# Performance work log

Hardware: AMD Instinct MI355X
Metric: run time of the kernel (lower is better)

Reference implementation:

```python
import jax, jax.numpy as jnp
import numpy as np
import math

EPS = 1e-5


def _layernorm(x, gamma, beta):
    mu = jnp.mean(x, axis=-1, keepdims=True)
    var = jnp.var(x, axis=-1, keepdims=True)
    return (x - mu) * jax.lax.rsqrt(var + EPS) * gamma + beta


def _quantum_head(x, theta_rx):
    # RX(x_i) then RX(theta_i) on wire i == RX(x_i + theta_i); product state,
    # CNOT ring is a Z-basis permutation => <Z_j> = prod_{i in S_j} cos(a_i)
    # with S_j = {0..j} for j>=1 (chain of CNOT(i,i+1)) and S_0 = {1..7}
    # (final CNOT(7,0) makes b0 = b1^...^b7).
    c = jnp.cos(x + theta_rx)                       # (B,S,8)
    cp = jnp.cumprod(c, axis=-1)                    # prefix products c0..cj
    z0 = jnp.prod(c[..., 1:], axis=-1, keepdims=True)
    return jnp.concatenate([z0, cp[..., 1:]], axis=-1)  # (B,S,8)


def _quantum_ffn(x, theta_ry):
    # RX(x_i) |0>, then RY(theta_i), measure Z: <Z_i> = cos(theta_i) * cos(x_i)
    return jnp.cos(theta_ry) * jnp.cos(x)


def setup_inputs() -> dict:
    key = jax.random.key(0)
    ks = jax.random.split(key, 6)
    B, S, E, F = 16, 2048, 8, 512
    return {
        'x': jax.random.normal(ks[0], (B, S, E), jnp.float32),
        'theta_rx': jax.random.normal(ks[1], (E,), jnp.float32),
        'w_out': jax.random.normal(ks[2], (E, E), jnp.float32) / math.sqrt(E),
        'theta_ry': jax.random.normal(ks[3], (E,), jnp.float32),
        'w1': jax.random.normal(ks[4], (F, E), jnp.float32) / math.sqrt(E),
        'b1': jnp.zeros((F,), jnp.float32),
        'w2': jax.random.normal(ks[5], (E, F), jnp.float32) / math.sqrt(F),
        'b2': jnp.zeros((E,), jnp.float32),
        'gamma1': jnp.ones((E,), jnp.float32),
        'beta1': jnp.zeros((E,), jnp.float32),
        'gamma2': jnp.ones((E,), jnp.float32),
        'beta2': jnp.zeros((E,), jnp.float32),
    }


def reference(x, theta_rx, w_out, theta_ry, w1, b1, w2, b2,
              gamma1, beta1, gamma2, beta2):
    B, S, E = x.shape
    H = 2
    D = E // H
    # --- quantum multi-head attention (shared head => q == k == v) ---
    z = _quantum_head(x, theta_rx)                       # (B,S,E)
    qh = z.reshape(B, S, H, D).transpose(0, 2, 1, 3)     # (B,H,S,D)
    scores = jnp.einsum('bhqd,bhkd->bhqk', qh, qh) / math.sqrt(D)
    attn = jax.nn.softmax(scores, axis=-1)
    out = jnp.einsum('bhqk,bhkd->bhqd', attn, qh)        # (B,H,S,D)
    out = out.transpose(0, 2, 1, 3).reshape(B, S, E)
    attn_out = out @ w_out.T                             # out_proj, no bias
    x1 = _layernorm(x + attn_out, gamma1, beta1)
    # --- quantum feed-forward ---
    zf = _quantum_ffn(x1, theta_ry)                      # (B,S,E)
    h = zf @ w1.T + b1                                   # (B,S,F)
    ffn_out = jax.nn.relu(h) @ w2.T + b2                 # (B,S,E)
    return _layernorm(x1 + ffn_out, gamma2, beta2)
```

## Files before the change

### kernel.cpp

```cpp
#include <hip/hip_runtime.h>
#include <math.h>
#include <utility>

#define NB 16
#define NS 2048
#define NE 8
#define NH 2
#define NF 512
#define DEG 6
#define NMONO 210
#define KPB 64
#define NCHUNK 32
#define PHI_LD 66
#define QPB 128
#define LNEPS 1e-5f
#define PART_STRIDE (5 * NMONO)

typedef float f32x2 __attribute__((ext_vector_type(2)));
typedef _Float16 h2 __attribute__((ext_vector_type(2)));

#if defined(__has_builtin)
# if __has_builtin(__builtin_amdgcn_fdot2)
#  define FDOT2(a,b,c) __builtin_amdgcn_fdot2((a),(b),(c),false)
# endif
#endif
#ifndef FDOT2
static __device__ __forceinline__ float fdot2_sw(h2 a, h2 b, float c) {
    return c + (float)a.x * (float)b.x + (float)a.y * (float)b.y;
}
# define FDOT2(a,b,c) fdot2_sw((a),(b),(c))
#endif

constexpr float ACOEF_C[7] = {0.99994459f, 2.00308514f, 2.00174650f,
                              1.30890404f, 0.65803033f, 0.31441604f, 0.10241921f};

constexpr int mono_e(int idx) {
    int i = 0;
    for (int e0 = 0; e0 <= DEG; ++e0)
        for (int e1 = 0; e1 <= DEG - e0; ++e1)
            for (int e2 = 0; e2 <= DEG - e0 - e1; ++e2)
                for (int e3 = 0; e3 <= DEG - e0 - e1 - e2; ++e3) {
                    if (i == idx) return (e0 << 12) | (e1 << 8) | (e2 << 4) | e3;
                    ++i;
                }
    return 0;
}
constexpr float mfact(int n) { float r = 1.f; for (int i = 2; i <= n; ++i) r *= (float)i; return r; }
constexpr float mono_c(int idx) {
    const int E = mono_e(idx);
    const int e0 = E >> 12, e1 = (E >> 8) & 15, e2 = (E >> 4) & 15, e3 = E & 15;
    const int d = e0 + e1 + e2 + e3;
    return ACOEF_C[d] * (mfact(d) / (mfact(e0) * mfact(e1) * mfact(e2) * mfact(e3)));
}

template <int BEG, class F, int... Is>
__device__ __forceinline__ void sf_impl(F f, std::integer_sequence<int, Is...>) {
    (f(std::integral_constant<int, BEG + Is>{}), ...);
}
template <int BEG, int END, class F>
__device__ __forceinline__ void static_for(F f) {
    sf_impl<BEG>(f, std::make_integer_sequence<int, END - BEG>{});
}

template <int BEG, int END>
__device__ __forceinline__ void phi_body(_Float16* __restrict__ Phi, int lane,
                                         const float (&pw0)[7], const float (&pw1)[7],
                                         const float (&pw2)[7], const float (&pw3)[7]) {
    static_for<BEG, END>([&](auto Ic) {
        constexpr int idx = Ic.value;
        constexpr int E = mono_e(idx);
        constexpr float C = mono_c(idx);
        const float v = C * (pw0[E >> 12] * pw1[(E >> 8) & 15]) *
                            (pw2[(E >> 4) & 15] * pw3[E & 15]);
        Phi[idx * PHI_LD + lane] = (_Float16)v;
    });
}

__global__ __launch_bounds__(256, 4)
void k1_moments(const float* __restrict__ x, const float* __restrict__ theta_rx,
                float* __restrict__ ws) {
    __shared__ _Float16 Phi[NMONO * PHI_LD];
    __shared__ __align__(16) _Float16 kvh[KPB / 2][8];
    __shared__ float th_s[8];

    const int t = threadIdx.x, bid = blockIdx.x;
    const int kc = bid & 31, h = (bid >> 5) & 1, b = bid >> 6;

    if (t < 8) th_s[t] = theta_rx[t];
    __syncthreads();

    const int lane = t & 63, wq = t >> 6;
    {
        const float* xr = x + ((size_t)b * NS + kc * KPB + lane) * NE;
        const float4 v0 = *reinterpret_cast<const float4*>(xr);
        const float4 v1 = *reinterpret_cast<const float4*>(xr + 4);
        const float c0 = __cosf(v0.x + th_s[0]), c1 = __cosf(v0.y + th_s[1]);
        const float c2 = __cosf(v0.z + th_s[2]), c3 = __cosf(v0.w + th_s[3]);
        const float c4 = __cosf(v1.x + th_s[4]), c5 = __cosf(v1.y + th_s[5]);
        const float c6 = __cosf(v1.z + th_s[6]), c7 = __cosf(v1.w + th_s[7]);
        const float p1 = c0*c1, p2 = p1*c2, p3 = p2*c3, p4 = p3*c4;
        const float p5 = p4*c5, p6 = p5*c6, p7 = p6*c7;
        float k0, k1v, k2v, k3v;
        if (h == 0) {
            const float s6 = c7*c6, s5 = s6*c5, s4 = s5*c4, s3 = s4*c3, s2 = s3*c2;
            k0 = s2*c1; k1v = p1; k2v = p2; k3v = p3;
        } else {
            k0 = p4; k1v = p5; k2v = p6; k3v = p7;
        }
        if (t < 64) {
            const int j = t >> 1, par = t & 1;
            kvh[j][0 + par] = (_Float16)k0;  kvh[j][2 + par] = (_Float16)k1v;
            kvh[j][4 + par] = (_Float16)k2v; kvh[j][6 + par] = (_Float16)k3v;
        }
        float pw0[7], pw1[7], pw2[7], pw3[7];
        pw0[0] = pw1[0] = pw2[0] = pw3[0] = 1.f;
        #pragma unroll
        for (int i = 1; i <= DEG; ++i) {
            pw0[i] = pw0[i-1] * k0;  pw1[i] = pw1[i-1] * k1v;
            pw2[i] = pw2[i-1] * k2v; pw3[i] = pw3[i-1] * k3v;
        }
        switch (wq) {
            case 0: phi_body<0,   53 >(Phi, lane, pw0, pw1, pw2, pw3); break;
            case 1: phi_body<53,  106>(Phi, lane, pw0, pw1, pw2, pw3); break;
            case 2: phi_body<106, 159>(Phi, lane, pw0, pw1, pw2, pw3); break;
            default: phi_body<159, 210>(Phi, lane, pw0, pw1, pw2, pw3); break;
        }
    }
    __syncthreads();

    if (t < NMONO) {
        const h2 one2 = {(_Float16)1.f, (_Float16)1.f};
        float a0 = 0.f, a1 = 0.f, a2 = 0.f, a3 = 0.f, a4 = 0.f;
        #pragma unroll 8
        for (int j = 0; j < KPB / 2; ++j) {
            const h2 phi2 = *reinterpret_cast<const h2*>(&Phi[t * PHI_LD + 2 * j]);
            const float4 kv4 = *reinterpret_cast<const float4*>(&kvh[j][0]);
            const h2 kA = __builtin_bit_cast(h2, kv4.x);
            const h2 kB = __builtin_bit_cast(h2, kv4.y);
            const h2 kC = __builtin_bit_cast(h2, kv4.z);
            const h2 kD = __builtin_bit_cast(h2, kv4.w);
            a0 = FDOT2(phi2, kA, a0);
            a1 = FDOT2(phi2, kB, a1);
            a2 = FDOT2(phi2, kC, a2);
            a3 = FDOT2(phi2, kD, a3);
            a4 = FDOT2(phi2, one2, a4);
        }
        float* dst = ws + (size_t)bid * PART_STRIDE;
        dst[0 * NMONO + t] = a0;
        dst[1 * NMONO + t] = a1;
        dst[2 * NMONO + t] = a2;
        dst[3 * NMONO + t] = a3;
        dst[4 * NMONO + t] = a4;
    }
}

template <int BEG, int END>
__device__ __forceinline__ void p2_body2(const float4* __restrict__ Mn,
                                         const float* __restrict__ Md, int base,
                                         const float (&pwA)[4][7], const float (&pwB)[4][7],
                                         f32x2& a01A, f32x2& a23A, float& adA,
                                         f32x2& a01B, f32x2& a23B, float& adB) {
    static_for<BEG, END>([&](auto Ic) {
        constexpr int idx = Ic.value;
        constexpr int E = mono_e(idx);
        constexpr int e0 = E >> 12, e1 = (E >> 8) & 15, e2 = (E >> 4) & 15, e3 = E & 15;
        const float4 mv = Mn[base + idx];
        const float  md = Md[base + idx];
        const f32x2 m01 = {mv.x, mv.y}, m23 = {mv.z, mv.w};
        const float PA = (pwA[0][e0] * pwA[1][e1]) * (pwA[2][e2] * pwA[3][e3]);
        const float PB = (pwB[0][e0] * pwB[1][e1]) * (pwB[2][e2] * pwB[3][e3]);
        a01A += PA * m01;  a23A += PA * m23;  adA += PA * md;
        a01B += PB * m01;  a23B += PB * m23;  adB += PB * md;
    });
}

__global__ __launch_bounds__(1024)
void k2_main(const float* __restrict__ x, const float* __restrict__ theta_rx,
             const float* __restrict__ w_out, const float* __restrict__ theta_ry,
             const float* __restrict__ w1, const float* __restrict__ b1,
             const float* __restrict__ w2, const float* __restrict__ b2,
             const float* __restrict__ g1, const float* __restrict__ be1,
             const float* __restrict__ g2, const float* __restrict__ be2,
             const float* __restrict__ ws, float* __restrict__ out) {
    __shared__ float4 Mn_lds[2 * NMONO];
    __shared__ float  Md_lds[2 * NMONO];
    __shared__ float  z_c[8][QPB];
    __shared__ float  x1_c[8][QPB];
    __shared__ float  zf_c[8][QPB];
    __shared__ float  attn_c[8][QPB];
    __shared__ float  part_a[4][256][5];
    __shared__ float  part_f[8][QPB][9];
    __shared__ float  w1_s[NF][NE];
    __shared__ float  w2t_s[NF][NE];
    __shared__ float  b1_s[NF];
    __shared__ float  wout_s[NE][NE];
    __shared__ float  th_s[8], cry_s[8], g1_s[8], be1_s[8], g2_s[8], be2_s[8], b2_s[8];

    const int t = threadIdx.x, bid = blockIdx.x;
    const int b = bid >> 4, qc = bid & 15;

    if (t < 2 * NMONO) {
        const int h = (t >= NMONO) ? 1 : 0;
        const int a = t - h * NMONO;
        const float* src = ws + (size_t)((b * 2 + h) * NCHUNK) * PART_STRIDE;
        float s0 = 0.f, s1 = 0.f, s2 = 0.f, s3 = 0.f, s4 = 0.f;
        #pragma unroll 4
        for (int kc = 0; kc < NCHUNK; ++kc) {
            const float* p = src + (size_t)kc * PART_STRIDE;
            s0 += p[0 * NMONO + a]; s1 += p[1 * NMONO + a];
            s2 += p[2 * NMONO + a]; s3 += p[3 * NMONO + a];
            s4 += p[4 * NMONO + a];
        }
        Mn_lds[t] = make_float4(s0, s1, s2, s3);
        Md_lds[t] = s4;
    }

    for (int i = t; i < NF * NE; i += 1024) {
        ((float*)w1_s)[i] = w1[i];
        const int e = i >> 9, f = i & (NF - 1);
        w2t_s[f][e] = w2[i];
    }
    if (t < NF) b1_s[t] = b1[t];
    if (t < NE * NE) ((float*)wout_s)[t] = w_out[t];
    if (t < 8) {
        th_s[t]  = theta_rx[t];
        cry_s[t] = __cosf(theta_ry[t]);
        g1_s[t]  = g1[t];  be1_s[t] = be1[t];
        g2_s[t]  = g2[t];  be2_s[t] = be2[t];
        b2_s[t]  = b2[t];
    }
    __syncthreads();

    if (t < QPB) {
        const float* xr = x + ((size_t)b * NS + qc * QPB + t) * NE;
        const float4 v0 = *reinterpret_cast<const float4*>(xr);
        const float4 v1 = *reinterpret_cast<const float4*>(xr + 4);
        const float c0 = __cosf(v0.x + th_s[0]), c1 = __cosf(v0.y + th_s[1]);
        const float c2 = __cosf(v0.z + th_s[2]), c3 = __cosf(v0.w + th_s[3]);
        const float c4 = __cosf(v1.x + th_s[4]), c5 = __cosf(v1.y + th_s[5]);
        const float c6 = __cosf(v1.z + th_s[6]), c7 = __cosf(v1.w + th_s[7]);
        const float p1 = c0*c1, p2 = p1*c2, p3 = p2*c3, p4 = p3*c4;
        const float p5 = p4*c5, p6 = p5*c6, p7 = p6*c7;
        const float s6 = c7*c6, s5 = s6*c5, s4 = s5*c4, s3 = s4*c3, s2 = s3*c2;
        z_c[0][t] = s2*c1; z_c[1][t] = p1; z_c[2][t] = p2; z_c[3][t] = p3;
        z_c[4][t] = p4;    z_c[5][t] = p5; z_c[6][t] = p6; z_c[7][t] = p7;
    }
    __syncthreads();

    if (t < 512) {
        const int w = t >> 6, l = t & 63;
        const int g = w >> 1, h = w & 1;
        const int rA = l, rB = l + 64;
        float pwA[4][7], pwB[4][7];
        #pragma unroll
        for (int d = 0; d < 4; ++d) {
            const float uA = z_c[h*4+d][rA] * 0.25f;
            const float uB = z_c[h*4+d][rB] * 0.25f;
            pwA[d][0] = 1.f; pwB[d][0] = 1.f;
            #pragma unroll
            for (int i = 1; i <= DEG; ++i) {
                pwA[d][i] = pwA[d][i-1] * uA;
                pwB[d][i] = pwB[d][i-1] * uB;
            }
        }
        f32x2 a01A = {0.f,0.f}, a23A = {0.f,0.f}, a01B = {0.f,0.f}, a23B = {0.f,0.f};
        float adA = 0.f, adB = 0.f;
        const int base = h * NMONO;
        switch (g) {
            case 0: p2_body2<0,   53 >(Mn_lds, Md_lds, base, pwA, pwB, a01A, a23A, adA, a01B, a23B, adB); break;
            case 1: p2_body2<53,  106>(Mn_lds, Md_lds, base, pwA, pwB, a01A, a23A, adA, a01B, a23B, adB); break;
            case 2: p2_body2<106, 159>(Mn_lds, Md_lds, base, pwA, pwB, a01A, a23A, adA, a01B, a23B, adB); break;
            default: p2_body2<159, 210>(Mn_lds, Md_lds, base, pwA, pwB, a01A, a23A, adA, a01B, a23B, adB); break;
        }
        float* pa = &part_a[g][h * 128 + rA][0];
        pa[0] = a01A.x; pa[1] = a01A.y; pa[2] = a23A.x; pa[3] = a23A.y; pa[4] = adA;
        float* pb = &part_a[g][h * 128 + rB][0];
        pb[0] = a01B.x; pb[1] = a01B.y; pb[2] = a23B.x; pb[3] = a23B.y; pb[4] = adB;
    }
    __syncthreads();

    if (t < 256) {
        const int h = t >> 7, r = t & 127;
        float n0 = 0.f, n1 = 0.f, n2 = 0.f, n3 = 0.f, dd = 0.f;
        #pragma unroll
        for (int g = 0; g < 4; ++g) {
            const float* pa = &part_a[g][t][0];
            n0 += pa[0]; n1 += pa[1]; n2 += pa[2]; n3 += pa[3]; dd += pa[4];
        }
        const float inv = 1.0f / dd;
        attn_c[h*4+0][r] = n0 * inv; attn_c[h*4+1][r] = n1 * inv;
        attn_c[h*4+2][r] = n2 * inv; attn_c[h*4+3][r] = n3 * inv;
    }
    __syncthreads();

    if (t < QPB) {
        float av[NE];
        #pragma unroll
        for (int e = 0; e < NE; ++e) av[e] = attn_c[e][t];
        float y[NE];
        #pragma unroll
        for (int e = 0; e < NE; ++e) {
            float acc = 0.f;
            #pragma unroll
            for (int k = 0; k < NE; ++k) acc += av[k] * wout_s[e][k];
            y[e] = acc;
        }
        const float* xr = x + ((size_t)b * NS + qc * QPB + t) * NE;
        const float4 xv0 = *reinterpret_cast<const float4*>(xr);
        const float4 xv1 = *reinterpret_cast<const float4*>(xr + 4);
        float t1[NE];
        t1[0] = xv0.x + y[0]; t1[1] = xv0.y + y[1]; t1[2] = xv0.z + y[2]; t1[3] = xv0.w + y[3];
        t1[4] = xv1.x + y[4]; t1[5] = xv1.y + y[5]; t1[6] = xv1.z + y[6]; t1[7] = xv1.w + y[7];
        float mu = 0.f;
        #pragma unroll
        for (int e = 0; e < NE; ++e) mu += t1[e];
        mu *= 0.125f;
        float var = 0.f;
        #pragma unroll
        for (int e = 0; e < NE; ++e) { const float d = t1[e] - mu; var += d * d; }
        var *= 0.125f;
        const float inv1 = rsqrtf(var + LNEPS);
        #pragma unroll
        for (int e = 0; e < NE; ++e) {
            const float x1e = (t1[e] - mu) * inv1 * g1_s[e] + be1_s[e];
            x1_c[e][t] = x1e;
            zf_c[e][t] = cry_s[e] * __cosf(x1e);
        }
    }
    __syncthreads();

    if (t < 256) {
        const int fs = t >> 5;
        const int rr = t & 31;
        f32x2 zf01[4], zf23[4], zf45[4], zf67[4];
        #pragma unroll
        for (int k = 0; k < 4; ++k) {
            const int row = rr + 32 * k;
            zf01[k] = (f32x2){zf_c[0][row], zf_c[1][row]};
            zf23[k] = (f32x2){zf_c[2][row], zf_c[3][row]};
            zf45[k] = (f32x2){zf_c[4][row], zf_c[5][row]};
            zf67[k] = (f32x2){zf_c[6][row], zf_c[7][row]};
        }
        f32x2 a01[4] = {}, a23[4] = {}, a45[4] = {}, a67[4] = {};
        #pragma unroll 4
        for (int i = 0; i < 64; ++i) {
            const int f = fs * 64 + i;
            const float4 wa = *reinterpret_cast<const float4*>(&w1_s[f][0]);
            const float4 wb = *reinterpret_cast<const float4*>(&w1_s[f][4]);
            const float bb = b1_s[f];
            const float4 ua = *reinterpret_cast<const float4*>(&w2t_s[f][0]);
            const float4 ub = *reinterpret_cast<const float4*>(&w2t_s[f][4]);
            const f32x2 wa01 = {wa.x, wa.y}, wa23 = {wa.z, wa.w};
            const f32x2 wb45 = {wb.x, wb.y}, wb67 = {wb.z, wb.w};
            const f32x2 ua01 = {ua.x, ua.y}, ua23 = {ua.z, ua.w};
            const f32x2 ub45 = {ub.x, ub.y}, ub67 = {ub.z, ub.w};
            #pragma unroll
            for (int k = 0; k < 4; ++k) {
                const f32x2 ha = zf01[k] * wa01 + zf23[k] * wa23;
                const f32x2 hb = zf45[k] * wb45 + zf67[k] * wb67;
                float hv = bb + ha.x + ha.y + hb.x + hb.y;
                hv = fmaxf(hv, 0.f);
                a01[k] += hv * ua01;  a23[k] += hv * ua23;
                a45[k] += hv * ub45;  a67[k] += hv * ub67;
            }
        }
        #pragma unroll
        for (int k = 0; k < 4; ++k) {
            const int row = rr + 32 * k;
            float* pf = &part_f[fs][row][0];
            pf[0] = a01[k].x; pf[1] = a01[k].y; pf[2] = a23[k].x; pf[3] = a23[k].y;
            pf[4] = a45[k].x; pf[5] = a45[k].y; pf[6] = a67[k].x; pf[7] = a67[k].y;
        }
    }
    __syncthreads();

    {
        const int e = t >> 7, r = t & 127;
        float s = 0.f;
        #pragma unroll
        for (int fs = 0; fs < 8; ++fs) s += part_f[fs][r][e];
        zf_c[e][r] = x1_c[e][r] + s + b2_s[e];
    }
    __syncthreads();

    if (t < QPB) {
        float t2[NE];
        #pragma unroll
        for (int e = 0; e < NE; ++e) t2[e] = zf_c[e][t];
        float mu = 0.f;
        #pragma unroll
        for (int e = 0; e < NE; ++e) mu += t2[e];
        mu *= 0.125f;
        float var = 0.f;
        #pragma unroll
        for (int e = 0; e < NE; ++e) { const float d = t2[e] - mu; var += d * d; }
        var *= 0.125f;
        const float inv2 = rsqrtf(var + LNEPS);
        float o[NE];
        #pragma unroll
        for (int e = 0; e < NE; ++e) o[e] = (t2[e] - mu) * inv2 * g2_s[e] + be2_s[e];
        float4* o4 = reinterpret_cast<float4*>(out + ((size_t)b * NS + qc * QPB + t) * NE);
        o4[0] = make_float4(o[0], o[1], o[2], o[3]);
        o4[1] = make_float4(o[4], o[5], o[6], o[7]);
    }
}

extern "C" void kernel_launch(void* const* d_in, const int* in_sizes, int n_in,
                              void* d_out, int out_size, void* d_ws, size_t ws_size,
                              hipStream_t stream) {
    const float* x        = (const float*)d_in[0];
    const float* theta_rx = (const float*)d_in[1];
    const float* w_out    = (const float*)d_in[2];
    const float* theta_ry = (const float*)d_in[3];
    const float* w1       = (const float*)d_in[4];
    const float* b1       = (const float*)d_in[5];
    const float* w2       = (const float*)d_in[6];
    const float* b2       = (const float*)d_in[7];
    const float* g1       = (const float*)d_in[8];
    const float* be1      = (const float*)d_in[9];
    const float* g2       = (const float*)d_in[10];
    const float* be2      = (const float*)d_in[11];
    float* out = (float*)d_out;
    float* ws  = (float*)d_ws;

    k1_moments<<<dim3(NB * NH * NCHUNK), dim3(256), 0, stream>>>(x, theta_rx, ws);
    k2_main<<<dim3(NB * (NS / QPB)), dim3(1024), 0, stream>>>(
        x, theta_rx, w_out, theta_ry, w1, b1, w2, b2, g1, be1, g2, be2, ws, out);
}
```

Baseline: 35.60 us.

## Fuse moment and main kernels into one cooperative kernel with grid sync

Merges the moment-computation kernel and the main kernel into a single cooperative launch of 256 blocks. Each 1024-thread block first handles four moment tasks, with phase-A and phase-B shared memory overlaid in a union, then waits on a grid-wide barrier before the attention/FFN phase. Weight loading into shared memory now happens before the moment phase, so it no longer sits after the workspace reduction. This removes one kernel launch and the gap between the two kernels, in exchange for a grid sync and a requirement that all 256 blocks be co-resident.

```diff
diff --git a/kernel.cpp b/kernel.cpp
--- a/kernel.cpp
+++ b/kernel.cpp
@@ -1,6 +1,9 @@
 #include <hip/hip_runtime.h>
+#include <hip/hip_cooperative_groups.h>
 #include <math.h>
 #include <utility>
+
+namespace cg = cooperative_groups;
 
 #define NB 16
 #define NS 2048
@@ -74,84 +77,6 @@
                             (pw2[(E >> 4) & 15] * pw3[E & 15]);
         Phi[idx * PHI_LD + lane] = (_Float16)v;
     });
-}
-
-__global__ __launch_bounds__(256, 4)
-void k1_moments(const float* __restrict__ x, const float* __restrict__ theta_rx,
-                float* __restrict__ ws) {
-    __shared__ _Float16 Phi[NMONO * PHI_LD];
-    __shared__ __align__(16) _Float16 kvh[KPB / 2][8];
-    __shared__ float th_s[8];
-
-    const int t = threadIdx.x, bid = blockIdx.x;
-    const int kc = bid & 31, h = (bid >> 5) & 1, b = bid >> 6;
-
-    if (t < 8) th_s[t] = theta_rx[t];
-    __syncthreads();
-
-    const int lane = t & 63, wq = t >> 6;
-    {
-        const float* xr = x + ((size_t)b * NS + kc * KPB + lane) * NE;
-        const float4 v0 = *reinterpret_cast<const float4*>(xr);
-        const float4 v1 = *reinterpret_cast<const float4*>(xr + 4);
-        const float c0 = __cosf(v0.x + th_s[0]), c1 = __cosf(v0.y + th_s[1]);
-        const float c2 = __cosf(v0.z + th_s[2]), c3 = __cosf(v0.w + th_s[3]);
-        const float c4 = __cosf(v1.x + th_s[4]), c5 = __cosf(v1.y + th_s[5]);
-        const float c6 = __cosf(v1.z + th_s[6]), c7 = __cosf(v1.w + th_s[7]);
-        const float p1 = c0*c1, p2 = p1*c2, p3 = p2*c3, p4 = p3*c4;
-        const float p5 = p4*c5, p6 = p5*c6, p7 = p6*c7;
-        float k0, k1v, k2v, k3v;
-        if (h == 0) {
-            const float s6 = c7*c6, s5 = s6*c5, s4 = s5*c4, s3 = s4*c3, s2 = s3*c2;
-            k0 = s2*c1; k1v = p1; k2v = p2; k3v = p3;
-        } else {
-            k0 = p4; k1v = p5; k2v = p6; k3v = p7;
-        }
-        if (t < 64) {
-            const int j = t >> 1, par = t & 1;
-            kvh[j][0 + par] = (_Float16)k0;  kvh[j][2 + par] = (_Float16)k1v;
-            kvh[j][4 + par] = (_Float16)k2v; kvh[j][6 + par] = (_Float16)k3v;
-        }
-        float pw0[7], pw1[7], pw2[7], pw3[7];
-        pw0[0] = pw1[0] = pw2[0] = pw3[0] = 1.f;
-        #pragma unroll
-        for (int i = 1; i <= DEG; ++i) {
-            pw0[i] = pw0[i-1] * k0;  pw1[i] = pw1[i-1] * k1v;
-            pw2[i] = pw2[i-1] * k2v; pw3[i] = pw3[i-1] * k3v;
-        }
-        switch (wq) {
-            case 0: phi_body<0,   53 >(Phi, lane, pw0, pw1, pw2, pw3); break;
-            case 1: phi_body<53,  106>(Phi, lane, pw0, pw1, pw2, pw3); break;
-            case 2: phi_body<106, 159>(Phi, lane, pw0, pw1, pw2, pw3); break;
-            default: phi_body<159, 210>(Phi, lane, pw0, pw1, pw2, pw3); break;
-        }
-    }
-    __syncthreads();
-
-    if (t < NMONO) {
-        const h2 one2 = {(_Float16)1.f, (_Float16)1.f};
-        float a0 = 0.f, a1 = 0.f, a2 = 0.f, a3 = 0.f, a4 = 0.f;
-        #pragma unroll 8
-        for (int j = 0; j < KPB / 2; ++j) {
-            const h2 phi2 = *reinterpret_cast<const h2*>(&Phi[t * PHI_LD + 2 * j]);
-            const float4 kv4 = *reinterpret_cast<const float4*>(&kvh[j][0]);
-            const h2 kA = __builtin_bit_cast(h2, kv4.x);
-            const h2 kB = __builtin_bit_cast(h2, kv4.y);
-            const h2 kC = __builtin_bit_cast(h2, kv4.z);
-            const h2 kD = __builtin_bit_cast(h2, kv4.w);
-            a0 = FDOT2(phi2, kA, a0);
-            a1 = FDOT2(phi2, kB, a1);
-            a2 = FDOT2(phi2, kC, a2);
-            a3 = FDOT2(phi2, kD, a3);
-            a4 = FDOT2(phi2, one2, a4);
-        }
-        float* dst = ws + (size_t)bid * PART_STRIDE;
-        dst[0 * NMONO + t] = a0;
-        dst[1 * NMONO + t] = a1;
-        dst[2 * NMONO + t] = a2;
-        dst[3 * NMONO + t] = a3;
-        dst[4 * NMONO + t] = a4;
-    }
 }
 
 template <int BEG, int END>
@@ -174,29 +99,131 @@
     });
 }
 
+struct PhaseA_sm {
+    _Float16 Phi[4][NMONO * PHI_LD];
+    _Float16 kvh[4][KPB / 2][8];
+};
+struct PhaseB_sm {
+    float4 Mn[2 * NMONO];
+    float  Md[2 * NMONO];
+    float  z[NE][QPB];
+    float  x1[NE][QPB];
+    float  zf[NE][QPB];
+    float  attn[NE][QPB];
+    float  part_a[4][256][5];
+    float  part_f[8][QPB][9];
+};
+union USm { PhaseA_sm a; PhaseB_sm b; };
+
 __global__ __launch_bounds__(1024)
-void k2_main(const float* __restrict__ x, const float* __restrict__ theta_rx,
-             const float* __restrict__ w_out, const float* __restrict__ theta_ry,
-             const float* __restrict__ w1, const float* __restrict__ b1,
-             const float* __restrict__ w2, const float* __restrict__ b2,
-             const float* __restrict__ g1, const float* __restrict__ be1,
-             const float* __restrict__ g2, const float* __restrict__ be2,
-             const float* __restrict__ ws, float* __restrict__ out) {
-    __shared__ float4 Mn_lds[2 * NMONO];
-    __shared__ float  Md_lds[2 * NMONO];
-    __shared__ float  z_c[8][QPB];
-    __shared__ float  x1_c[8][QPB];
-    __shared__ float  zf_c[8][QPB];
-    __shared__ float  attn_c[8][QPB];
-    __shared__ float  part_a[4][256][5];
-    __shared__ float  part_f[8][QPB][9];
-    __shared__ float  w1_s[NF][NE];
-    __shared__ float  w2t_s[NF][NE];
-    __shared__ float  b1_s[NF];
-    __shared__ float  wout_s[NE][NE];
-    __shared__ float  th_s[8], cry_s[8], g1_s[8], be1_s[8], g2_s[8], be2_s[8], b2_s[8];
+void fused_qtb(const float* __restrict__ x, const float* __restrict__ theta_rx,
+               const float* __restrict__ w_out, const float* __restrict__ theta_ry,
+               const float* __restrict__ w1, const float* __restrict__ b1,
+               const float* __restrict__ w2, const float* __restrict__ b2,
+               const float* __restrict__ g1, const float* __restrict__ be1,
+               const float* __restrict__ g2, const float* __restrict__ be2,
+               float* __restrict__ ws, float* __restrict__ out) {
+    __shared__ USm sm;
+    __shared__ float w1_s[NF][NE];
+    __shared__ float w2t_s[NF][NE];
+    __shared__ float b1_s[NF];
+    __shared__ float wout_s[NE][NE];
+    __shared__ float th_s[8], cry_s[8], g1_s[8], be1_s[8], g2_s[8], be2_s[8], b2_s[8];
 
     const int t = threadIdx.x, bid = blockIdx.x;
+
+    for (int i = t; i < NF * NE; i += 1024) {
+        ((float*)w1_s)[i] = w1[i];
+        const int e = i >> 9, f = i & (NF - 1);
+        w2t_s[f][e] = w2[i];
+    }
+    if (t < NF) b1_s[t] = b1[t];
+    if (t < NE * NE) ((float*)wout_s)[t] = w_out[t];
+    if (t < 8) {
+        th_s[t]  = theta_rx[t];
+        cry_s[t] = __cosf(theta_ry[t]);
+        g1_s[t]  = g1[t];  be1_s[t] = be1[t];
+        g2_s[t]  = g2[t];  be2_s[t] = be2[t];
+        b2_s[t]  = b2[t];
+    }
+    __syncthreads();
+
+    {
+        const int g = t >> 8, tt = t & 255;
+        const int tk = bid * 4 + g;
+        const int kc = tk & 31, h = (tk >> 5) & 1, bb = tk >> 6;
+        const int lane = tt & 63, wq = tt >> 6;
+
+        const float* xr = x + ((size_t)bb * NS + kc * KPB + lane) * NE;
+        const float4 v0 = *reinterpret_cast<const float4*>(xr);
+        const float4 v1 = *reinterpret_cast<const float4*>(xr + 4);
+        const float c0 = __cosf(v0.x + th_s[0]), c1 = __cosf(v0.y + th_s[1]);
+        const float c2 = __cosf(v0.z + th_s[2]), c3 = __cosf(v0.w + th_s[3]);
+        const float c4 = __cosf(v1.x + th_s[4]), c5 = __cosf(v1.y + th_s[5]);
+        const float c6 = __cosf(v1.z + th_s[6]), c7 = __cosf(v1.w + th_s[7]);
+        const float p1 = c0*c1, p2 = p1*c2, p3 = p2*c3, p4 = p3*c4;
+        const float p5 = p4*c5, p6 = p5*c6, p7 = p6*c7;
+        float k0, k1v, k2v, k3v;
+        if (h == 0) {
+            const float s6 = c7*c6, s5 = s6*c5, s4 = s5*c4, s3 = s4*c3, s2 = s3*c2;
+            k0 = s2*c1; k1v = p1; k2v = p2; k3v = p3;
+        } else {
+            k0 = p4; k1v = p5; k2v = p6; k3v = p7;
+        }
+        if (tt < 64) {
+            const int j = tt >> 1, par = tt & 1;
+            sm.a.kvh[g][j][0 + par] = (_Float16)k0;  sm.a.kvh[g][j][2 + par] = (_Float16)k1v;
+            sm.a.kvh[g][j][4 + par] = (_Float16)k2v; sm.a.kvh[g][j][6 + par] = (_Float16)k3v;
+        }
+        float pw0[7], pw1[7], pw2[7], pw3[7];
+        pw0[0] = pw1[0] = pw2[0] = pw3[0] = 1.f;
+        #pragma unroll
+        for (int i = 1; i <= DEG; ++i) {
+            pw0[i] = pw0[i-1] * k0;  pw1[i] = pw1[i-1] * k1v;
+            pw2[i] = pw2[i-1] * k2v; pw3[i] = pw3[i-1] * k3v;
+        }
+        _Float16* PhiG = &sm.a.Phi[g][0];
+        switch (wq) {
+            case 0: phi_body<0,   53 >(PhiG, lane, pw0, pw1, pw2, pw3); break;
+            case 1: phi_body<53,  106>(PhiG, lane, pw0, pw1, pw2, pw3); break;
+            case 2: phi_body<106, 159>(PhiG, lane, pw0, pw1, pw2, pw3); break;
+            default: phi_body<159, 210>(PhiG, lane, pw0, pw1, pw2, pw3); break;
+        }
+    }
+    __syncthreads();
+
+    {
+        const int g = t >> 8, tt = t & 255;
+        const int tk = bid * 4 + g;
+        if (tt < NMONO) {
+            const h2 one2 = {(_Float16)1.f, (_Float16)1.f};
+            const _Float16* PhiG = &sm.a.Phi[g][0];
+            float a0 = 0.f, a1 = 0.f, a2 = 0.f, a3 = 0.f, a4 = 0.f;
+            #pragma unroll 8
+            for (int j = 0; j < KPB / 2; ++j) {
+                const h2 phi2 = *reinterpret_cast<const h2*>(&PhiG[tt * PHI_LD + 2 * j]);
+                const float4 kv4 = *reinterpret_cast<const float4*>(&sm.a.kvh[g][j][0]);
+                const h2 kA = __builtin_bit_cast(h2, kv4.x);
+                const h2 kB = __builtin_bit_cast(h2, kv4.y);
+                const h2 kC = __builtin_bit_cast(h2, kv4.z);
+                const h2 kD = __builtin_bit_cast(h2, kv4.w);
+                a0 = FDOT2(phi2, kA, a0);
+                a1 = FDOT2(phi2, kB, a1);
+                a2 = FDOT2(phi2, kC, a2);
+                a3 = FDOT2(phi2, kD, a3);
+                a4 = FDOT2(phi2, one2, a4);
+            }
+            float* dst = ws + (size_t)tk * PART_STRIDE;
+            dst[0 * NMONO + tt] = a0;
+            dst[1 * NMONO + tt] = a1;
+            dst[2 * NMONO + tt] = a2;
+            dst[3 * NMONO + tt] = a3;
+            dst[4 * NMONO + tt] = a4;
+        }
+    }
+
+    cg::this_grid().sync();
+
     const int b = bid >> 4, qc = bid & 15;
 
     if (t < 2 * NMONO) {
@@ -211,23 +238,8 @@
             s2 += p[2 * NMONO + a]; s3 += p[3 * NMONO + a];
             s4 += p[4 * NMONO + a];
         }
-        Mn_lds[t] = make_float4(s0, s1, s2, s3);
-        Md_lds[t] = s4;
-    }
-
-    for (int i = t; i < NF * NE; i += 1024) {
-        ((float*)w1_s)[i] = w1[i];
-        const int e = i >> 9, f = i & (NF - 1);
-        w2t_s[f][e] = w2[i];
-    }
-    if (t < NF) b1_s[t] = b1[t];
-    if (t < NE * NE) ((float*)wout_s)[t] = w_out[t];
-    if (t < 8) {
-        th_s[t]  = theta_rx[t];
-        cry_s[t] = __cosf(theta_ry[t]);
-        g1_s[t]  = g1[t];  be1_s[t] = be1[t];
-        g2_s[t]  = g2[t];  be2_s[t] = be2[t];
-        b2_s[t]  = b2[t];
+        sm.b.Mn[t] = make_float4(s0, s1, s2, s3);
+        sm.b.Md[t] = s4;
     }
     __syncthreads();
 
@@ -242,8 +254,8 @@
         const float p1 = c0*c1, p2 = p1*c2, p3 = p2*c3, p4 = p3*c4;
         const float p5 = p4*c5, p6 = p5*c6, p7 = p6*c7;
         const float s6 = c7*c6, s5 = s6*c5, s4 = s5*c4, s3 = s4*c3, s2 = s3*c2;
-        z_c[0][t] = s2*c1; z_c[1][t] = p1; z_c[2][t] = p2; z_c[3][t] = p3;
-        z_c[4][t] = p4;    z_c[5][t] = p5; z_c[6][t] = p6; z_c[7][t] = p7;
+        sm.b.z[0][t] = s2*c1; sm.b.z[1][t] = p1; sm.b.z[2][t] = p2; sm.b.z[3][t] = p3;
+        sm.b.z[4][t] = p4;    sm.b.z[5][t] = p5; sm.b.z[6][t] = p6; sm.b.z[7][t] = p7;
     }
     __syncthreads();
 
@@ -254,8 +266,8 @@
         float pwA[4][7], pwB[4][7];
         #pragma unroll
         for (int d = 0; d < 4; ++d) {
-            const float uA = z_c[h*4+d][rA] * 0.25f;
-            const float uB = z_c[h*4+d][rB] * 0.25f;
+            const float uA = sm.b.z[h*4+d][rA] * 0.25f;
+            const float uB = sm.b.z[h*4+d][rB] * 0.25f;
             pwA[d][0] = 1.f; pwB[d][0] = 1.f;
             #pragma unroll
             for (int i = 1; i <= DEG; ++i) {
@@ -267,14 +279,14 @@
         float adA = 0.f, adB = 0.f;
         const int base = h * NMONO;
         switch (g) {
-            case 0: p2_body2<0,   53 >(Mn_lds, Md_lds, base, pwA, pwB, a01A, a23A, adA, a01B, a23B, adB); break;
-            case 1: p2_body2<53,  106>(Mn_lds, Md_lds, base, pwA, pwB, a01A, a23A, adA, a01B, a23B, adB); break;
-            case 2: p2_body2<106, 159>(Mn_lds, Md_lds, base, pwA, pwB, a01A, a23A, adA, a01B, a23B, adB); break;
-            default: p2_body2<159, 210>(Mn_lds, Md_lds, base, pwA, pwB, a01A, a23A, adA, a01B, a23B, adB); break;
-        }
-        float* pa = &part_a[g][h * 128 + rA][0];
+            case 0: p2_body2<0,   53 >(sm.b.Mn, sm.b.Md, base, pwA, pwB, a01A, a23A, adA, a01B, a23B, adB); break;
+            case 1: p2_body2<53,  106>(sm.b.Mn, sm.b.Md, base, pwA, pwB, a01A, a23A, adA, a01B, a23B, adB); break;
+            case 2: p2_body2<106, 159>(sm.b.Mn, sm.b.Md, base, pwA, pwB, a01A, a23A, adA, a01B, a23B, adB); break;
+            default: p2_body2<159, 210>(sm.b.Mn, sm.b.Md, base, pwA, pwB, a01A, a23A, adA, a01B, a23B, adB); break;
+        }
+        float* pa = &sm.b.part_a[g][h * 128 + rA][0];
         pa[0] = a01A.x; pa[1] = a01A.y; pa[2] = a23A.x; pa[3] = a23A.y; pa[4] = adA;
-        float* pb = &part_a[g][h * 128 + rB][0];
+        float* pb = &sm.b.part_a[g][h * 128 + rB][0];
         pb[0] = a01B.x; pb[1] = a01B.y; pb[2] = a23B.x; pb[3] = a23B.y; pb[4] = adB;
     }
     __syncthreads();
@@ -284,19 +296,19 @@
         float n0 = 0.f, n1 = 0.f, n2 = 0.f, n3 = 0.f, dd = 0.f;
         #pragma unroll
         for (int g = 0; g < 4; ++g) {
-            const float* pa = &part_a[g][t][0];
+            const float* pa = &sm.b.part_a[g][t][0];
             n0 += pa[0]; n1 += pa[1]; n2 += pa[2]; n3 += pa[3]; dd += pa[4];
         }
         const float inv = 1.0f / dd;
-        attn_c[h*4+0][r] = n0 * inv; attn_c[h*4+1][r] = n1 * inv;
-        attn_c[h*4+2][r] = n2 * inv; attn_c[h*4+3][r] = n3 * inv;
+        sm.b.attn[h*4+0][r] = n0 * inv; sm.b.attn[h*4+1][r] = n1 * inv;
+        sm.b.attn[h*4+2][r] = n2 * inv; sm.b.attn[h*4+3][r] = n3 * inv;
     }
     __syncthreads();
 
     if (t < QPB) {
         float av[NE];
         #pragma unroll
-        for (int e = 0; e < NE; ++e) av[e] = attn_c[e][t];
+        for (int e = 0; e < NE; ++e) av[e] = sm.b.attn[e][t];
         float y[NE];
         #pragma unroll
         for (int e = 0; e < NE; ++e) {
@@ -323,8 +335,8 @@
         #pragma unroll
         for (int e = 0; e < NE; ++e) {
             const float x1e = (t1[e] - mu) * inv1 * g1_s[e] + be1_s[e];
-            x1_c[e][t] = x1e;
-            zf_c[e][t] = cry_s[e] * __cosf(x1e);
+            sm.b.x1[e][t] = x1e;
+            sm.b.zf[e][t] = cry_s[e] * __cosf(x1e);
         }
     }
     __syncthreads();
@@ -336,10 +348,10 @@
         #pragma unroll
         for (int k = 0; k < 4; ++k) {
             const int row = rr + 32 * k;
-            zf01[k] = (f32x2){zf_c[0][row], zf_c[1][row]};
-            zf23[k] = (f32x2){zf_c[2][row], zf_c[3][row]};
-            zf45[k] = (f32x2){zf_c[4][row], zf_c[5][row]};
-            zf67[k] = (f32x2){zf_c[6][row], zf_c[7][row]};
+            zf01[k] = (f32x2){sm.b.zf[0][row], sm.b.zf[1][row]};
+            zf23[k] = (f32x2){sm.b.zf[2][row], sm.b.zf[3][row]};
+            zf45[k] = (f32x2){sm.b.zf[4][row], sm.b.zf[5][row]};
+            zf67[k] = (f32x2){sm.b.zf[6][row], sm.b.zf[7][row]};
         }
         f32x2 a01[4] = {}, a23[4] = {}, a45[4] = {}, a67[4] = {};
         #pragma unroll 4
@@ -367,7 +379,7 @@
         #pragma unroll
         for (int k = 0; k < 4; ++k) {
             const int row = rr + 32 * k;
-            float* pf = &part_f[fs][row][0];
+            float* pf = &sm.b.part_f[fs][row][0];
             pf[0] = a01[k].x; pf[1] = a01[k].y; pf[2] = a23[k].x; pf[3] = a23[k].y;
             pf[4] = a45[k].x; pf[5] = a45[k].y; pf[6] = a67[k].x; pf[7] = a67[k].y;
         }
@@ -378,15 +390,15 @@
         const int e = t >> 7, r = t & 127;
         float s = 0.f;
         #pragma unroll
-        for (int fs = 0; fs < 8; ++fs) s += part_f[fs][r][e];
-        zf_c[e][r] = x1_c[e][r] + s + b2_s[e];
+        for (int fs = 0; fs < 8; ++fs) s += sm.b.part_f[fs][r][e];
+        sm.b.zf[e][r] = sm.b.x1[e][r] + s + b2_s[e];
     }
     __syncthreads();
 
     if (t < QPB) {
         float t2[NE];
         #pragma unroll
-        for (int e = 0; e < NE; ++e) t2[e] = zf_c[e][t];
+        for (int e = 0; e < NE; ++e) t2[e] = sm.b.zf[e][t];
         float mu = 0.f;
         #pragma unroll
         for (int e = 0; e < NE; ++e) mu += t2[e];
@@ -423,7 +435,8 @@
     float* out = (float*)d_out;
     float* ws  = (float*)d_ws;
 
-    k1_moments<<<dim3(NB * NH * NCHUNK), dim3(256), 0, stream>>>(x, theta_rx, ws);
-    k2_main<<<dim3(NB * (NS / QPB)), dim3(1024), 0, stream>>>(
-        x, theta_rx, w_out, theta_ry, w1, b1, w2, b2, g1, be1, g2, be2, ws, out);
-}
+    void* args[] = {&x, &theta_rx, &w_out, &theta_ry, &w1, &b1, &w2, &b2,
+                    &g1, &be1, &g2, &be2, &ws, &out};
+    hipLaunchCooperativeKernel((const void*)fused_qtb, dim3(NB * (NS / QPB)),
+                               dim3(1024), args, 0, stream);
+}
```

Result: slower. 81.29 us (+128.4%).

## Halve queries per block in main kernel, use 512-thread blocks and merge phases

Applied to the files above, without the earlier changes.

The main kernel now handles 64 queries per block with 512 threads instead of 128 queries with 1024 threads, which doubles the grid to 512 blocks. Each thread evaluates one query row in the moment-polynomial phase instead of two. Weight staging and the per-row cosine computation run in the same phase as the moment reduction, which removes a barrier, and the attention-normalisation step is folded into the out-projection threads. The aim is more blocks and occupancy across CUs. The cost is that each block re-reduces the moment partials and reloads the FFN weights, so this redundant global and LDS traffic doubles.

```diff
diff --git a/kernel.cpp b/kernel.cpp
--- a/kernel.cpp
+++ b/kernel.cpp
@@ -12,7 +12,8 @@
 #define KPB 64
 #define NCHUNK 32
 #define PHI_LD 66
-#define QPB 128
+#define QPB 64
+#define NTH2 512
 #define LNEPS 1e-5f
 #define PART_STRIDE (5 * NMONO)
 
@@ -155,26 +156,24 @@
 }
 
 template <int BEG, int END>
-__device__ __forceinline__ void p2_body2(const float4* __restrict__ Mn,
+__device__ __forceinline__ void p2_body1(const float4* __restrict__ Mn,
                                          const float* __restrict__ Md, int base,
-                                         const float (&pwA)[4][7], const float (&pwB)[4][7],
-                                         f32x2& a01A, f32x2& a23A, float& adA,
-                                         f32x2& a01B, f32x2& a23B, float& adB) {
+                                         const float (&pw)[4][7],
+                                         f32x2& a01, f32x2& a23, float& ad) {
     static_for<BEG, END>([&](auto Ic) {
         constexpr int idx = Ic.value;
         constexpr int E = mono_e(idx);
         constexpr int e0 = E >> 12, e1 = (E >> 8) & 15, e2 = (E >> 4) & 15, e3 = E & 15;
         const float4 mv = Mn[base + idx];
         const float  md = Md[base + idx];
-        const f32x2 m01 = {mv.x, mv.y}, m23 = {mv.z, mv.w};
-        const float PA = (pwA[0][e0] * pwA[1][e1]) * (pwA[2][e2] * pwA[3][e3]);
-        const float PB = (pwB[0][e0] * pwB[1][e1]) * (pwB[2][e2] * pwB[3][e3]);
-        a01A += PA * m01;  a23A += PA * m23;  adA += PA * md;
-        a01B += PB * m01;  a23B += PB * m23;  adB += PB * md;
+        const float P = (pw[0][e0] * pw[1][e1]) * (pw[2][e2] * pw[3][e3]);
+        a01 += P * (f32x2){mv.x, mv.y};
+        a23 += P * (f32x2){mv.z, mv.w};
+        ad  += P * md;
     });
 }
 
-__global__ __launch_bounds__(1024)
+__global__ __launch_bounds__(NTH2, 4)
 void k2_main(const float* __restrict__ x, const float* __restrict__ theta_rx,
              const float* __restrict__ w_out, const float* __restrict__ theta_ry,
              const float* __restrict__ w1, const float* __restrict__ b1,
@@ -187,18 +186,30 @@
     __shared__ float  z_c[8][QPB];
     __shared__ float  x1_c[8][QPB];
     __shared__ float  zf_c[8][QPB];
-    __shared__ float  attn_c[8][QPB];
-    __shared__ float  part_a[4][256][5];
-    __shared__ float  part_f[8][QPB][9];
+    __shared__ float  part_a[4][128][5];
+    __shared__ float  part_f[8][8][QPB];
     __shared__ float  w1_s[NF][NE];
     __shared__ float  w2t_s[NF][NE];
     __shared__ float  b1_s[NF];
     __shared__ float  wout_s[NE][NE];
-    __shared__ float  th_s[8], cry_s[8], g1_s[8], be1_s[8], g2_s[8], be2_s[8], b2_s[8];
+    __shared__ float  cry_s[8], g1_s[8], be1_s[8], g2_s[8], be2_s[8], b2_s[8];
 
     const int t = threadIdx.x, bid = blockIdx.x;
-    const int b = bid >> 4, qc = bid & 15;
-
+    const int b = bid >> 5, qc = bid & 31;
+
+    for (int i = t; i < NF * NE; i += NTH2) {
+        ((float*)w1_s)[i] = w1[i];
+        const int e = i >> 9, f = i & (NF - 1);
+        w2t_s[f][e] = w2[i];
+    }
+    b1_s[t] = b1[t];
+    if (t < NE * NE) ((float*)wout_s)[t] = w_out[t];
+    if (t < 8) {
+        cry_s[t] = __cosf(theta_ry[t]);
+        g1_s[t]  = g1[t];  be1_s[t] = be1[t];
+        g2_s[t]  = g2[t];  be2_s[t] = be2[t];
+        b2_s[t]  = b2[t];
+    }
     if (t < 2 * NMONO) {
         const int h = (t >= NMONO) ? 1 : 0;
         const int a = t - h * NMONO;
@@ -214,89 +225,64 @@
         Mn_lds[t] = make_float4(s0, s1, s2, s3);
         Md_lds[t] = s4;
     }
-
-    for (int i = t; i < NF * NE; i += 1024) {
-        ((float*)w1_s)[i] = w1[i];
-        const int e = i >> 9, f = i & (NF - 1);
-        w2t_s[f][e] = w2[i];
-    }
-    if (t < NF) b1_s[t] = b1[t];
-    if (t < NE * NE) ((float*)wout_s)[t] = w_out[t];
-    if (t < 8) {
-        th_s[t]  = theta_rx[t];
-        cry_s[t] = __cosf(theta_ry[t]);
-        g1_s[t]  = g1[t];  be1_s[t] = be1[t];
-        g2_s[t]  = g2[t];  be2_s[t] = be2[t];
-        b2_s[t]  = b2[t];
-    }
-    __syncthreads();
-
-    if (t < QPB) {
-        const float* xr = x + ((size_t)b * NS + qc * QPB + t) * NE;
+    if (t >= 448) {
+        const int r = t - 448;
+        const float* xr = x + ((size_t)b * NS + qc * QPB + r) * NE;
         const float4 v0 = *reinterpret_cast<const float4*>(xr);
         const float4 v1 = *reinterpret_cast<const float4*>(xr + 4);
-        const float c0 = __cosf(v0.x + th_s[0]), c1 = __cosf(v0.y + th_s[1]);
-        const float c2 = __cosf(v0.z + th_s[2]), c3 = __cosf(v0.w + th_s[3]);
-        const float c4 = __cosf(v1.x + th_s[4]), c5 = __cosf(v1.y + th_s[5]);
-        const float c6 = __cosf(v1.z + th_s[6]), c7 = __cosf(v1.w + th_s[7]);
+        const float4 ta = *reinterpret_cast<const float4*>(theta_rx);
+        const float4 tb = *reinterpret_cast<const float4*>(theta_rx + 4);
+        const float c0 = __cosf(v0.x + ta.x), c1 = __cosf(v0.y + ta.y);
+        const float c2 = __cosf(v0.z + ta.z), c3 = __cosf(v0.w + ta.w);
+        const float c4 = __cosf(v1.x + tb.x), c5 = __cosf(v1.y + tb.y);
+        const float c6 = __cosf(v1.z + tb.z), c7 = __cosf(v1.w + tb.w);
         const float p1 = c0*c1, p2 = p1*c2, p3 = p2*c3, p4 = p3*c4;
         const float p5 = p4*c5, p6 = p5*c6, p7 = p6*c7;
         const float s6 = c7*c6, s5 = s6*c5, s4 = s5*c4, s3 = s4*c3, s2 = s3*c2;
-        z_c[0][t] = s2*c1; z_c[1][t] = p1; z_c[2][t] = p2; z_c[3][t] = p3;
-        z_c[4][t] = p4;    z_c[5][t] = p5; z_c[6][t] = p6; z_c[7][t] = p7;
-    }
-    __syncthreads();
-
-    if (t < 512) {
-        const int w = t >> 6, l = t & 63;
+        z_c[0][r] = s2*c1; z_c[1][r] = p1; z_c[2][r] = p2; z_c[3][r] = p3;
+        z_c[4][r] = p4;    z_c[5][r] = p5; z_c[6][r] = p6; z_c[7][r] = p7;
+    }
+    __syncthreads();
+
+    {
+        const int w = t >> 6, r = t & 63;
         const int g = w >> 1, h = w & 1;
-        const int rA = l, rB = l + 64;
-        float pwA[4][7], pwB[4][7];
+        float pw[4][7];
         #pragma unroll
         for (int d = 0; d < 4; ++d) {
-            const float uA = z_c[h*4+d][rA] * 0.25f;
-            const float uB = z_c[h*4+d][rB] * 0.25f;
-            pwA[d][0] = 1.f; pwB[d][0] = 1.f;
+            const float u = z_c[h*4+d][r] * 0.25f;
+            pw[d][0] = 1.f;
             #pragma unroll
-            for (int i = 1; i <= DEG; ++i) {
-                pwA[d][i] = pwA[d][i-1] * uA;
-                pwB[d][i] = pwB[d][i-1] * uB;
-            }
-        }
-        f32x2 a01A = {0.f,0.f}, a23A = {0.f,0.f}, a01B = {0.f,0.f}, a23B = {0.f,0.f};
-        float adA = 0.f, adB = 0.f;
+            for (int i = 1; i <= DEG; ++i) pw[d][i] = pw[d][i-1] * u;
+        }
+        f32x2 a01 = {0.f,0.f}, a23 = {0.f,0.f};
+        float ad = 0.f;
         const int base = h * NMONO;
         switch (g) {
-            case 0: p2_body2<0,   53 >(Mn_lds, Md_lds, base, pwA, pwB, a01A, a23A, adA, a01B, a23B, adB); break;
-            case 1: p2_body2<53,  106>(Mn_lds, Md_lds, base, pwA, pwB, a01A, a23A, adA, a01B, a23B, adB); break;
-            case 2: p2_body2<106, 159>(Mn_lds, Md_lds, base, pwA, pwB, a01A, a23A, adA, a01B, a23B, adB); break;
-            default: p2_body2<159, 210>(Mn_lds, Md_lds, base, pwA, pwB, a01A, a23A, adA, a01B, a23B, adB); break;
-        }
-        float* pa = &part_a[g][h * 128 + rA][0];
-        pa[0] = a01A.x; pa[1] = a01A.y; pa[2] = a23A.x; pa[3] = a23A.y; pa[4] = adA;
-        float* pb = &part_a[g][h * 128 + rB][0];
-        pb[0] = a01B.x; pb[1] = a01B.y; pb[2] = a23B.x; pb[3] = a23B.y; pb[4] = adB;
-    }
-    __syncthreads();
-
-    if (t < 256) {
-        const int h = t >> 7, r = t & 127;
-        float n0 = 0.f, n1 = 0.f, n2 = 0.f, n3 = 0.f, dd = 0.f;
-        #pragma unroll
-        for (int g = 0; g < 4; ++g) {
-            const float* pa = &part_a[g][t][0];
-            n0 += pa[0]; n1 += pa[1]; n2 += pa[2]; n3 += pa[3]; dd += pa[4];
-        }
-        const float inv = 1.0f / dd;
-        attn_c[h*4+0][r] = n0 * inv; attn_c[h*4+1][r] = n1 * inv;
-        attn_c[h*4+2][r] = n2 * inv; attn_c[h*4+3][r] = n3 * inv;
+            case 0: p2_body1<0,   53 >(Mn_lds, Md_lds, base, pw, a01, a23, ad); break;
+            case 1: p2_body1<53,  106>(Mn_lds, Md_lds, base, pw, a01, a23, ad); break;
+            case 2: p2_body1<106, 159>(Mn_lds, Md_lds, base, pw, a01, a23, ad); break;
+            default: p2_body1<159, 210>(Mn_lds, Md_lds, base, pw, a01, a23, ad); break;
+        }
+        float* pa = &part_a[g][h * 64 + r][0];
+        pa[0] = a01.x; pa[1] = a01.y; pa[2] = a23.x; pa[3] = a23.y; pa[4] = ad;
     }
     __syncthreads();
 
     if (t < QPB) {
         float av[NE];
         #pragma unroll
-        for (int e = 0; e < NE; ++e) av[e] = attn_c[e][t];
+        for (int h = 0; h < 2; ++h) {
+            float n0 = 0.f, n1 = 0.f, n2 = 0.f, n3 = 0.f, dd = 0.f;
+            #pragma unroll
+            for (int g = 0; g < 4; ++g) {
+                const float* pa = &part_a[g][h * 64 + t][0];
+                n0 += pa[0]; n1 += pa[1]; n2 += pa[2]; n3 += pa[3]; dd += pa[4];
+            }
+            const float inv = 1.0f / dd;
+            av[h*4+0] = n0 * inv; av[h*4+1] = n1 * inv;
+            av[h*4+2] = n2 * inv; av[h*4+3] = n3 * inv;
+        }
         float y[NE];
         #pragma unroll
         for (int e = 0; e < NE; ++e) {
@@ -332,16 +318,16 @@
     if (t < 256) {
         const int fs = t >> 5;
         const int rr = t & 31;
-        f32x2 zf01[4], zf23[4], zf45[4], zf67[4];
-        #pragma unroll
-        for (int k = 0; k < 4; ++k) {
+        f32x2 zf01[2], zf23[2], zf45[2], zf67[2];
+        #pragma unroll
+        for (int k = 0; k < 2; ++k) {
             const int row = rr + 32 * k;
             zf01[k] = (f32x2){zf_c[0][row], zf_c[1][row]};
             zf23[k] = (f32x2){zf_c[2][row], zf_c[3][row]};
             zf45[k] = (f32x2){zf_c[4][row], zf_c[5][row]};
             zf67[k] = (f32x2){zf_c[6][row], zf_c[7][row]};
         }
-        f32x2 a01[4] = {}, a23[4] = {}, a45[4] = {}, a67[4] = {};
+        f32x2 a01[2] = {}, a23[2] = {}, a45[2] = {}, a67[2] = {};
         #pragma unroll 4
         for (int i = 0; i < 64; ++i) {
             const int f = fs * 64 + i;
@@ -355,7 +341,7 @@
             const f32x2 ua01 = {ua.x, ua.y}, ua23 = {ua.z, ua.w};
             const f32x2 ub45 = {ub.x, ub.y}, ub67 = {ub.z, ub.w};
             #pragma unroll
-            for (int k = 0; k < 4; ++k) {
+            for (int k = 0; k < 2; ++k) {
                 const f32x2 ha = zf01[k] * wa01 + zf23[k] * wa23;
                 const f32x2 hb = zf45[k] * wb45 + zf67[k] * wb67;
                 float hv = bb + ha.x + ha.y + hb.x + hb.y;
@@ -365,20 +351,21 @@
             }
         }
         #pragma unroll
-        for (int k = 0; k < 4; ++k) {
+        for (int k = 0; k < 2; ++k) {
             const int row = rr + 32 * k;
-            float* pf = &part_f[fs][row][0];
-            pf[0] = a01[k].x; pf[1] = a01[k].y; pf[2] = a23[k].x; pf[3] = a23[k].y;
-            pf[4] = a45[k].x; pf[5] = a45[k].y; pf[6] = a67[k].x; pf[7] = a67[k].y;
+            part_f[fs][0][row] = a01[k].x; part_f[fs][1][row] = a01[k].y;
+            part_f[fs][2][row] = a23[k].x; part_f[fs][3][row] = a23[k].y;
+            part_f[fs][4][row] = a45[k].x; part_f[fs][5][row] = a45[k].y;
+            part_f[fs][6][row] = a67[k].x; part_f[fs][7][row] = a67[k].y;
         }
     }
     __syncthreads();
 
     {
-        const int e = t >> 7, r = t & 127;
+        const int e = t >> 6, r = t & 63;
         float s = 0.f;
         #pragma unroll
-        for (int fs = 0; fs < 8; ++fs) s += part_f[fs][r][e];
+        for (int fs = 0; fs < 8; ++fs) s += part_f[fs][e][r];
         zf_c[e][r] = x1_c[e][r] + s + b2_s[e];
     }
     __syncthreads();
@@ -424,6 +411,6 @@
     float* ws  = (float*)d_ws;
 
     k1_moments<<<dim3(NB * NH * NCHUNK), dim3(256), 0, stream>>>(x, theta_rx, ws);
-    k2_main<<<dim3(NB * (NS / QPB)), dim3(1024), 0, stream>>>(
+    k2_main<<<dim3(NB * (NS / QPB)), dim3(NTH2), 0, stream>>>(
         x, theta_rx, w_out, theta_ry, w1, b1, w2, b2, g1, be1, g2, be2, ws, out);
 }
```

Measured after the change: 37.98 us. +6.7%, slower.
